# Kernel tuning notes

Hardware: AMD Instinct MI355X
Metric: run time of the kernel (lower is better)

Reference implementation:

```python
import jax, jax.numpy as jnp
import numpy as np

B, S, T, H, V = 32, 64, 64, 512, 32000


def setup_inputs() -> dict:
    key = jax.random.key(0)
    ks = jax.random.split(key, 14)
    enc = jax.random.normal(ks[0], (B, S, H), jnp.float32)
    h0 = jax.random.normal(ks[1], (1, B, H), jnp.float32)
    # encoder padding mask: at least half of each row valid (avoids all -inf rows)
    src_len = jax.random.randint(ks[2], (B,), S // 2, S + 1)
    enc_mask = (jnp.arange(S)[None, :] < src_len[:, None])
    tgt = jax.random.randint(ks[3], (B, T), 0, V)
    fra_len = jax.random.randint(ks[4], (B,), 1, T + 1).at[0].set(T)
    s = 1.0 / np.sqrt(H)
    emb = jax.random.normal(ks[5], (V, H), jnp.float32) * s
    W_ih = jax.random.uniform(ks[6], (3 * H, H), jnp.float32, -s, s)
    W_hh = jax.random.uniform(ks[7], (3 * H, H), jnp.float32, -s, s)
    b_ih = jax.random.uniform(ks[8], (3 * H,), jnp.float32, -s, s)
    b_hh = jax.random.uniform(ks[9], (3 * H,), jnp.float32, -s, s)
    W_cc = jax.random.uniform(ks[10], (H, 2 * H), jnp.float32, -s, s)
    b_cc = jnp.zeros((H,), jnp.float32)
    W_out = jax.random.uniform(ks[11], (V, H), jnp.float32, -s, s)
    b_out = jnp.zeros((V,), jnp.float32)
    return {"all_encoder_hidden_states": enc, "initial_decoder_hidden_state": h0,
            "encoder_output_mask": enc_mask, "target_input": tgt, "fra_length": fra_len,
            "embedding": emb, "W_ih": W_ih, "W_hh": W_hh, "b_ih": b_ih, "b_hh": b_hh,
            "W_cc": W_cc, "b_cc": b_cc, "W_out": W_out, "b_out": b_out}


def reference(all_encoder_hidden_states, initial_decoder_hidden_state, encoder_output_mask,
              target_input, fra_length, embedding, W_ih, W_hh, b_ih, b_hh,
              W_cc, b_cc, W_out, b_out):
    enc = all_encoder_hidden_states            # [B,S,H]
    mask = encoder_output_mask                 # [B,S] bool
    xs = embedding[target_input].transpose(1, 0, 2)  # [T,B,H]
    ts = jnp.arange(xs.shape[0])

    def step(h, inp):                          # h: [B,H]
        x, t = inp
        gx = x @ W_ih.T + b_ih                 # [B,3H]
        gh = h @ W_hh.T + b_hh
        gxr, gxz, gxn = jnp.split(gx, 3, axis=-1)
        ghr, ghz, ghn = jnp.split(gh, 3, axis=-1)
        r = jax.nn.sigmoid(gxr + ghr)
        z = jax.nn.sigmoid(gxz + ghz)
        n = jnp.tanh(gxn + r * ghn)
        h_new = (1.0 - z) * n + z * h          # torch GRU update
        # Luong dot-product attention
        scores = jnp.einsum('bsh,bh->bs', enc, h_new)
        scores = jnp.where(mask, scores, -jnp.inf)
        alphas = jax.nn.softmax(scores, axis=-1)
        ctx = jnp.einsum('bs,bsh->bh', alphas, enc)
        ho = jnp.tanh(jnp.concatenate([ctx, h_new], axis=-1) @ W_cc.T + b_cc)
        logit = ho @ W_out.T + b_out           # [B,V]
        active = (t < fra_length)[:, None]
        h_next = jnp.where(active, h_new, h)   # freeze finished sequences
        return h_next, logit

    _, logits = jax.lax.scan(step, initial_decoder_hidden_state[0], (xs, ts))
    logits = logits.transpose(1, 0, 2)          # [B,T,V]
    return jax.nn.log_softmax(logits, axis=-1)
```

## Files before the change

### kernel.cpp

```cpp
#include <hip/hip_runtime.h>

static constexpr int Bn = 32, Sn = 64, Tn = 64, Hn = 512, Vn = 32000;
static constexpr int H3 = 1536;
static constexpr int NBLK = 64;

typedef __attribute__((ext_vector_type(8))) short bf16x8;
typedef __attribute__((ext_vector_type(4))) float f32x4;

__device__ __forceinline__ short f2bf(float f) {
    unsigned u = __float_as_uint(f);
    u += 0x7FFFu + ((u >> 16) & 1u);
    return (short)(u >> 16);
}
__device__ __forceinline__ float bf2f(short s) {
    return __uint_as_float(((unsigned)(unsigned short)s) << 16);
}

__device__ __forceinline__ void gload16(const void* g, void* l) {
    __builtin_amdgcn_global_load_lds(
        (const __attribute__((address_space(1))) unsigned int*)g,
        (__attribute__((address_space(3))) unsigned int*)l, 16, 0, 0);
}

__global__ __launch_bounds__(128) void k_gather(const int* __restrict__ tgt,
                                                const float* __restrict__ emb,
                                                short* __restrict__ Xb) {
    int m = blockIdx.x;
    int c = threadIdx.x * 4;
    const float4 v = *(const float4*)(emb + (long)tgt[m] * Hn + c);
    short4 o; o.x = f2bf(v.x); o.y = f2bf(v.y); o.z = f2bf(v.z); o.w = f2bf(v.w);
    *(short4*)(Xb + (long)m * Hn + c) = o;
}

__global__ __launch_bounds__(256) void k_cvt(const float* __restrict__ src, int src_ld, int src_off,
                                             short* __restrict__ dst, long total4) {
    for (long i = (long)blockIdx.x * 256 + threadIdx.x; i < total4; i += (long)gridDim.x * 256) {
        long e = i * 4;
        long r = e >> 9; int c = (int)(e & 511);
        const float4 v = *(const float4*)(src + r * (long)src_ld + src_off + c);
        short4 o; o.x = f2bf(v.x); o.y = f2bf(v.y); o.z = f2bf(v.z); o.w = f2bf(v.w);
        *(short4*)(dst + e) = o;
    }
}

__global__ __launch_bounds__(256) void k_gemm_bf16(const short* __restrict__ A, int lda,
                                                   const short* __restrict__ Bm, int ldb,
                                                   const float* __restrict__ bias,
                                                   float* __restrict__ C, int ldc, int K) {
    __shared__ short lA[4096];
    __shared__ short lB[4096];
    const int tid = threadIdx.x;
    const int row0 = blockIdx.y * 128;
    const int col0 = blockIdx.x * 128;
    const int lane = tid & 63;
    const int w = tid >> 6;
    const int wr = w >> 1, wc = w & 1;
    const int g = lane >> 4, rr = lane & 15;

    f32x4 acc[4][4];
    for (int m = 0; m < 4; ++m)
        for (int n = 0; n < 4; ++n)
            for (int q = 0; q < 4; ++q) acc[m][n][q] = 0.f;

    for (int kk = 0; kk < K; kk += 32) {
        for (int p = 0; p < 2; ++p) {
            int u = p * 256 + tid;
            int kg = u >> 7, r = u & 127;
            gload16(A + (long)(row0 + r) * lda + kk + kg * 8, &lA[u * 8]);
            gload16(Bm + (long)(col0 + r) * ldb + kk + kg * 8, &lB[u * 8]);
        }
        __syncthreads();
        bf16x8 av[4], bv[4];
        for (int m = 0; m < 4; ++m)
            av[m] = *(const bf16x8*)&lA[(g * 128 + wr * 64 + m * 16 + rr) * 8];
        for (int n = 0; n < 4; ++n)
            bv[n] = *(const bf16x8*)&lB[(g * 128 + wc * 64 + n * 16 + rr) * 8];
        for (int m = 0; m < 4; ++m)
            for (int n = 0; n < 4; ++n)
                acc[m][n] = __builtin_amdgcn_mfma_f32_16x16x32_bf16(av[m], bv[n], acc[m][n], 0, 0, 0);
        __syncthreads();
    }

    for (int n = 0; n < 4; ++n) {
        int gc = col0 + wc * 64 + n * 16 + rr;
        float bb = bias ? bias[gc] : 0.f;
        for (int m = 0; m < 4; ++m) {
            int gr = row0 + wr * 64 + m * 16 + g * 4;
            for (int q = 0; q < 4; ++q)
                C[(long)(gr + q) * ldc + gc] = acc[m][n][q] + bb;
        }
    }
}

struct WSm2 {
    short h_all[Bn * Hn];
    short hnb[2][Bn * Hn];
    float gh_sl[3 * 16 * 32];
    float y1l[Bn * 16];
    int   flen[Bn];
};
struct BSm2 {
    short encl[Sn * 520];
    short encWl[Sn * Hn];
    float scp[8][64];
    float al[64];
    short hnf[Hn];
};
union USm2 { WSm2 w; BSm2 b; };

__device__ __forceinline__ void sig_flag(unsigned* slot, unsigned val) {
    asm volatile("s_waitcnt vmcnt(0)" ::: "memory");
    __syncthreads();
    if (threadIdx.x == 0)
        __hip_atomic_store(slot, val, __ATOMIC_RELAXED, __HIP_MEMORY_SCOPE_AGENT);
}
__device__ __forceinline__ void wait_flags32(const unsigned* base, unsigned need) {
    if (threadIdx.x < 32) {
        while (__hip_atomic_load(base + threadIdx.x * 32, __ATOMIC_RELAXED, __HIP_MEMORY_SCOPE_AGENT) < need)
            __builtin_amdgcn_s_sleep(1);
    }
    __syncthreads();
}

__global__ __launch_bounds__(512, 1) void k_seq(
    const float* __restrict__ GX, const float* __restrict__ enc,
    const void* __restrict__ maskp, const int* __restrict__ fra,
    const float* __restrict__ h0,
    const short* __restrict__ Whh_b, const float* __restrict__ b_hh,
    const short* __restrict__ Wcc2_b, const float* __restrict__ b_cc,
    const float* __restrict__ encW,
    short* __restrict__ ho_out,
    unsigned long long* __restrict__ hn_pub,
    float* __restrict__ y1_pub,
    unsigned* __restrict__ flags)
{
    __shared__ __align__(16) USm2 sm;
    const int bid = blockIdx.x;
    const int tid = threadIdx.x;
    const int wv = tid >> 6, lane = tid & 63;
    unsigned* flagW = flags;
    unsigned* flagB = flags + 1024;

    if (bid < Bn) {
        bf16x8 afr[16];
        if (wv < 6) {
            const int g = wv >> 1;
            const int row = g * 512 + bid * 16 + (lane & 15);
            #pragma unroll
            for (int k = 0; k < 16; ++k)
                afr[k] = *(const bf16x8*)(Whh_b + (long)row * 512 + k * 32 + (lane >> 4) * 8);
        } else {
            const int row = bid * 16 + (lane & 15);
            #pragma unroll
            for (int k = 0; k < 16; ++k)
                afr[k] = *(const bf16x8*)(Wcc2_b + (long)row * 512 + k * 32 + (lane >> 4) * 8);
        }
        if (tid < Bn) sm.w.flen[tid] = fra[tid];
        #pragma unroll
        for (int it = 0; it < 8; ++it) {
            const int idx2 = it * 512 + tid;
            const int b = idx2 >> 7, ci2 = idx2 & 127;
            const int j0 = ci2 * 4;
            const int soff = b * 512 + ((((ci2 >> 1)) ^ (b & 7)) << 3) + (ci2 & 1) * 4;
            const float4 v = *(const float4*)(h0 + b * 512 + j0);
            unsigned long long pk = (unsigned long long)(unsigned short)f2bf(v.x)
                                  | ((unsigned long long)(unsigned short)f2bf(v.y) << 16)
                                  | ((unsigned long long)(unsigned short)f2bf(v.z) << 32)
                                  | ((unsigned long long)(unsigned short)f2bf(v.w) << 48);
            *(unsigned long long*)&sm.w.h_all[soff] = pk;
        }

        const int eb = tid >> 4, jj = tid & 15;
        float h_carry = h0[eb * 512 + bid * 16 + jj];
        const int flen_e = fra[eb];

        for (int t = 0; t <= Tn + 1; ++t) {
            float gxr = 0.f, gxz = 0.f, gxn = 0.f;
            if (t < Tn) {
                const long base = (long)(eb * Tn + t) * H3 + bid * 16 + jj;
                gxr = GX[base]; gxz = GX[base + 512]; gxn = GX[base + 1024];
            }
            if (t >= 1 && t <= Tn) {
                wait_flags32(flagW, (unsigned)t);
                const unsigned long long* src = hn_pub + ((t - 1) & 1) * 4096;
                short* dst = sm.w.hnb[(t - 1) & 1];
                #pragma unroll
                for (int it = 0; it < 8; ++it) {
                    const int idx2 = it * 512 + tid;
                    const int b = idx2 >> 7, ci2 = idx2 & 127;
                    const int soff = b * 512 + ((((ci2 >> 1)) ^ (b & 7)) << 3) + (ci2 & 1) * 4;
                    const unsigned long long v = __hip_atomic_load(src + idx2, __ATOMIC_RELAXED, __HIP_MEMORY_SCOPE_AGENT);
                    *(unsigned long long*)&dst[soff] = v;
                    if (t - 1 < sm.w.flen[b]) *(unsigned long long*)&sm.w.h_all[soff] = v;
                }
            }
            __syncthreads();
            if (t < Tn && wv < 6) {
                const int g = wv >> 1, n = wv & 1;
                const int bq = n * 16 + (lane & 15);
                f32x4 a0 = {0.f, 0.f, 0.f, 0.f}, a1 = {0.f, 0.f, 0.f, 0.f};
                #pragma unroll
                for (int k = 0; k < 8; ++k) {
                    const int c0 = k * 4 + (lane >> 4);
                    const int c1 = (k + 8) * 4 + (lane >> 4);
                    bf16x8 b0 = *(const bf16x8*)&sm.w.h_all[bq * 512 + ((c0 ^ (bq & 7)) << 3)];
                    bf16x8 b1 = *(const bf16x8*)&sm.w.h_all[bq * 512 + ((c1 ^ (bq & 7)) << 3)];
                    a0 = __builtin_amdgcn_mfma_f32_16x16x32_bf16(afr[k], b0, a0, 0, 0, 0);
                    a1 = __builtin_amdgcn_mfma_f32_16x16x32_bf16(afr[k + 8], b1, a1, 0, 0, 0);
                }
                const int r0 = (lane >> 4) * 4;
                #pragma unroll
                for (int q = 0; q < 4; ++q)
                    sm.w.gh_sl[g * 512 + (r0 + q) * 32 + bq] = a0[q] + a1[q];
            }
            __syncthreads();
            if (t < Tn) {
                const int j = bid * 16 + jj;
                const float ghr = sm.w.gh_sl[jj * 32 + eb]          + b_hh[j];
                const float ghz = sm.w.gh_sl[512 + jj * 32 + eb]    + b_hh[512 + j];
                const float ghn = sm.w.gh_sl[1024 + jj * 32 + eb]   + b_hh[1024 + j];
                const float r = 1.f / (1.f + expf(-(gxr + ghr)));
                const float z = 1.f / (1.f + expf(-(gxz + ghz)));
                const float nn = tanhf(gxn + r * ghn);
                const float hv = (1.f - z) * nn + z * h_carry;
                h_carry = (t < flen_e) ? hv : h_carry;
                int w32 = (int)(unsigned short)f2bf(hv);
                int n1 = __shfl_down(w32, 1);
                int n2 = __shfl_down(w32, 2);
                int n3 = __shfl_down(w32, 3);
                if ((jj & 3) == 0) {
                    unsigned long long pk = (unsigned long long)(unsigned)(w32 | (n1 << 16))
                                          | ((unsigned long long)(unsigned)(n2 | (n3 << 16)) << 32);
                    __hip_atomic_store(hn_pub + (t & 1) * 4096 + eb * 128 + bid * 4 + (jj >> 2), pk,
                                       __ATOMIC_RELAXED, __HIP_MEMORY_SCOPE_AGENT);
                }
                sig_flag(flagW + bid * 32, (unsigned)(t + 1));
            }
            if (t >= 2) {
                wait_flags32(flagB, (unsigned)(t - 1));
                sm.w.y1l[tid] = __hip_atomic_load(
                    y1_pub + ((t - 2) % 3) * (Bn * Hn) + (tid >> 4) * 512 + bid * 16 + (tid & 15),
                    __ATOMIC_RELAXED, __HIP_MEMORY_SCOPE_AGENT);
                __syncthreads();
                if (wv >= 6) {
                    const int n = wv - 6;
                    const int bq = n * 16 + (lane & 15);
                    const short* hsrc = sm.w.hnb[(t - 2) & 1];
                    f32x4 a0 = {0.f, 0.f, 0.f, 0.f}, a1 = {0.f, 0.f, 0.f, 0.f};
                    #pragma unroll
                    for (int k = 0; k < 8; ++k) {
                        const int c0 = k * 4 + (lane >> 4);
                        const int c1 = (k + 8) * 4 + (lane >> 4);
                        bf16x8 b0 = *(const bf16x8*)&hsrc[bq * 512 + ((c0 ^ (bq & 7)) << 3)];
                        bf16x8 b1 = *(const bf16x8*)&hsrc[bq * 512 + ((c1 ^ (bq & 7)) << 3)];
                        a0 = __builtin_amdgcn_mfma_f32_16x16x32_bf16(afr[k], b0, a0, 0, 0, 0);
                        a1 = __builtin_amdgcn_mfma_f32_16x16x32_bf16(afr[k + 8], b1, a1, 0, 0, 0);
                    }
                    const int r0 = (lane >> 4) * 4;
                    short4 o;
                    o.x = f2bf(tanhf(a0[0] + a1[0] + sm.w.y1l[bq * 16 + r0 + 0] + b_cc[bid * 16 + r0 + 0]));
                    o.y = f2bf(tanhf(a0[1] + a1[1] + sm.w.y1l[bq * 16 + r0 + 1] + b_cc[bid * 16 + r0 + 1]));
                    o.z = f2bf(tanhf(a0[2] + a1[2] + sm.w.y1l[bq * 16 + r0 + 2] + b_cc[bid * 16 + r0 + 2]));
                    o.w = f2bf(tanhf(a0[3] + a1[3] + sm.w.y1l[bq * 16 + r0 + 3] + b_cc[bid * 16 + r0 + 3]));
                    *(short4*)(ho_out + ((long)(bq * Tn + (t - 2))) * Hn + bid * 16 + r0) = o;
                }
            }
        }
    } else {
        const int b = bid - Bn;
        const unsigned w0 = ((const unsigned*)maskp)[0];
        const int mmode = (w0 == 1u) ? 0 : (w0 == 0x3F800000u ? 2 : 1);
        {
            const float* encb = enc + (long)b * (Sn * Hn);
            #pragma unroll
            for (int it = 0; it < 16; ++it) {
                int e = (it * 512 + tid) * 4;
                float4 v = *(const float4*)(encb + e);
                int s = e >> 9, k = e & 511;
                short4 o; o.x = f2bf(v.x); o.y = f2bf(v.y); o.z = f2bf(v.z); o.w = f2bf(v.w);
                *(short4*)(sm.b.encl + s * 520 + k) = o;
            }
        }
        {
            const float* ewb = encW + (long)b * (Sn * Hn);
            #pragma unroll
            for (int it = 0; it < 16; ++it) {
                int e = (it * 512 + tid) * 4;
                float4 v = *(const float4*)(ewb + e);
                short4 o; o.x = f2bf(v.x); o.y = f2bf(v.y); o.z = f2bf(v.z); o.w = f2bf(v.w);
                *(short4*)(sm.b.encWl + e) = o;
            }
        }

        for (int u = 0; u < Tn; ++u) {
            wait_flags32(flagW, (unsigned)(u + 1));
            if (tid < 128) {
                unsigned long long v = __hip_atomic_load(hn_pub + (u & 1) * 4096 + b * 128 + tid,
                                                         __ATOMIC_RELAXED, __HIP_MEMORY_SCOPE_AGENT);
                *(unsigned long long*)&sm.b.hnf[tid * 4] = v;
            }
            __syncthreads();
            {
                const int s = tid & 63, sub = tid >> 6;
                const short* erow = sm.b.encl + s * 520 + sub * 64;
                const short* hrow = sm.b.hnf + sub * 64;
                float p = 0.f;
                #pragma unroll
                for (int c8 = 0; c8 < 8; ++c8) {
                    bf16x8 ev = *(const bf16x8*)(erow + c8 * 8);
                    bf16x8 hv8 = *(const bf16x8*)(hrow + c8 * 8);
                    #pragma unroll
                    for (int e = 0; e < 8; ++e)
                        p += bf2f(ev[e]) * bf2f(hv8[e]);
                }
                sm.b.scp[sub][s] = p;
            }
            __syncthreads();
            if (tid < 64) {
                float v = 0.f;
                #pragma unroll
                for (int q = 0; q < 8; ++q) v += sm.b.scp[q][tid];
                bool mv;
                if (mmode == 0)      mv = ((const int*)maskp)[b * Sn + tid] != 0;
                else if (mmode == 1) mv = ((const unsigned char*)maskp)[b * Sn + tid] != 0;
                else                 mv = ((const float*)maskp)[b * Sn + tid] != 0.f;
                v = mv ? v : -__builtin_inff();
                float mx = v;
                for (int o = 1; o < 64; o <<= 1) mx = fmaxf(mx, __shfl_xor(mx, o));
                float e = expf(v - mx);
                float su = e;
                for (int o = 1; o < 64; o <<= 1) su += __shfl_xor(su, o);
                sm.b.al[tid] = e / su;
            }
            __syncthreads();
            {
                float acc = 0.f;
                #pragma unroll 8
                for (int s = 0; s < 64; ++s)
                    acc += sm.b.al[s] * bf2f(sm.b.encWl[s * 512 + tid]);
                __hip_atomic_store(y1_pub + (u % 3) * (Bn * Hn) + b * 512 + tid, acc,
                                   __ATOMIC_RELAXED, __HIP_MEMORY_SCOPE_AGENT);
            }
            sig_flag(flagB + b * 32, (unsigned)(u + 1));
        }
    }
}

__global__ __launch_bounds__(256) void k_logsoftmax(float* __restrict__ out) {
    const long row = blockIdx.x;
    float* p = out + row * (long)Vn;
    const int tid = threadIdx.x;
    __shared__ float redm[4];
    __shared__ float reds[4];

    float mx = -__builtin_inff(), sm = 0.f;
    for (int i = tid; i < Vn / 4; i += 256) {
        float4 v = *(const float4*)(p + i * 4);
        float e0 = v.x, e1 = v.y, e2 = v.z, e3 = v.w;
        float m01 = fmaxf(e0, e1), m23 = fmaxf(e2, e3);
        float ml = fmaxf(m01, m23);
        float nm = fmaxf(mx, ml);
        sm = sm * __expf(mx - nm) + __expf(e0 - nm) + __expf(e1 - nm) + __expf(e2 - nm) + __expf(e3 - nm);
        mx = nm;
    }
    for (int o = 1; o < 64; o <<= 1) {
        float omx = __shfl_xor(mx, o), osm = __shfl_xor(sm, o);
        float nm = fmaxf(mx, omx);
        sm = sm * __expf(mx - nm) + osm * __expf(omx - nm);
        mx = nm;
    }
    if ((tid & 63) == 0) { redm[tid >> 6] = mx; reds[tid >> 6] = sm; }
    __syncthreads();
    float gmx = fmaxf(fmaxf(redm[0], redm[1]), fmaxf(redm[2], redm[3]));
    float gsm = reds[0] * __expf(redm[0] - gmx) + reds[1] * __expf(redm[1] - gmx)
              + reds[2] * __expf(redm[2] - gmx) + reds[3] * __expf(redm[3] - gmx);
    const float lse = gmx + logf(gsm);

    for (int i = tid; i < Vn / 4; i += 256) {
        float4 v = *(const float4*)(p + i * 4);
        v.x -= lse; v.y -= lse; v.z -= lse; v.w -= lse;
        *(float4*)(p + i * 4) = v;
    }
}

extern "C" void kernel_launch(void* const* d_in, const int* in_sizes, int n_in,
                              void* d_out, int out_size, void* d_ws, size_t ws_size,
                              hipStream_t stream) {
    const float* enc   = (const float*)d_in[0];
    const float* h0    = (const float*)d_in[1];
    const void*  maskp = d_in[2];
    const int*   tgt   = (const int*)d_in[3];
    const int*   fra   = (const int*)d_in[4];
    const float* emb   = (const float*)d_in[5];
    const float* W_ih  = (const float*)d_in[6];
    const float* W_hh  = (const float*)d_in[7];
    const float* b_ih  = (const float*)d_in[8];
    const float* b_hh  = (const float*)d_in[9];
    const float* W_cc  = (const float*)d_in[10];
    const float* b_cc  = (const float*)d_in[11];
    const float* W_out = (const float*)d_in[12];
    const float* b_out = (const float*)d_in[13];
    float* out = (float*)d_out;

    char* ws = (char*)d_ws;
    float*    GX      = (float*)ws;   ws += (long)2048 * 1536 * 4;
    float*    encW_ws = (float*)ws;   ws += (long)2048 * 512 * 4;
    short*    Xb      = (short*)ws;   ws += (long)2048 * 512 * 2;
    short*    Wih_b   = (short*)ws;   ws += (long)1536 * 512 * 2;
    short*    Wout_b  = (short*)ws;   ws += (long)32000 * 512 * 2;
    short*    Whh_b   = (short*)ws;   ws += (long)1536 * 512 * 2;
    short*    Wc1_b   = (short*)ws;   ws += (long)512 * 512 * 2;
    short*    Wcc2_b  = (short*)ws;   ws += (long)512 * 512 * 2;
    short*    enc_b   = (short*)ws;   ws += (long)2048 * 512 * 2;
    short*    ho_b    = (short*)ws;   ws += (long)2048 * 512 * 2;
    unsigned long long* hn_pub = (unsigned long long*)ws; ws += (long)2 * 4096 * 8;
    float*    y1_pub  = (float*)ws;   ws += (long)3 * 32 * 512 * 4;
    unsigned* flags   = (unsigned*)ws; ws += 2 * 1024 * 4;

    k_gather<<<2048, 128, 0, stream>>>(tgt, emb, Xb);
    k_cvt<<<768, 256, 0, stream>>>(W_ih, 512, 0, Wih_b, (long)1536 * 512 / 4);
    k_cvt<<<4096, 256, 0, stream>>>(W_out, 512, 0, Wout_b, (long)32000 * 512 / 4);
    k_cvt<<<768, 256, 0, stream>>>(W_hh, 512, 0, Whh_b, (long)1536 * 512 / 4);
    k_cvt<<<256, 256, 0, stream>>>(W_cc, 1024, 0, Wc1_b, (long)512 * 512 / 4);
    k_cvt<<<256, 256, 0, stream>>>(W_cc, 1024, 512, Wcc2_b, (long)512 * 512 / 4);
    k_cvt<<<1024, 256, 0, stream>>>(enc, 512, 0, enc_b, (long)2048 * 512 / 4);

    k_gemm_bf16<<<dim3(12, 16), 256, 0, stream>>>(Xb, 512, Wih_b, 512, b_ih, GX, 1536, 512);
    k_gemm_bf16<<<dim3(4, 16), 256, 0, stream>>>(enc_b, 512, Wc1_b, 512, nullptr, encW_ws, 512, 512);

    hipMemsetAsync(flags, 0, 2 * 1024 * 4, stream);
    k_seq<<<NBLK, 512, 0, stream>>>(GX, enc, maskp, fra, h0,
                                    Whh_b, b_hh, Wcc2_b, b_cc, encW_ws,
                                    ho_b, hn_pub, y1_pub, flags);

    k_gemm_bf16<<<dim3(250, 16), 256, 0, stream>>>(ho_b, 512, Wout_b, 512, b_out, out, 32000, 512);

    k_logsoftmax<<<2048, 256, 0, stream>>>(out);
}
```

Before: 751.0 us.

## Move attention out of the recurrent kernel into batched post-recurrence kernels

```diff
diff --git a/kernel.cpp b/kernel.cpp
--- a/kernel.cpp
+++ b/kernel.cpp
@@ -2,7 +2,6 @@
 
 static constexpr int Bn = 32, Sn = 64, Tn = 64, Hn = 512, Vn = 32000;
 static constexpr int H3 = 1536;
-static constexpr int NBLK = 64;
 
 typedef __attribute__((ext_vector_type(8))) short bf16x8;
 typedef __attribute__((ext_vector_type(4))) float f32x4;
@@ -92,21 +91,57 @@
     }
 }
 
-struct WSm2 {
-    short h_all[Bn * Hn];
-    short hnb[2][Bn * Hn];
-    float gh_sl[3 * 16 * 32];
-    float y1l[Bn * 16];
-    int   flen[Bn];
-};
-struct BSm2 {
-    short encl[Sn * 520];
-    short encWl[Sn * Hn];
-    float scp[8][64];
-    float al[64];
-    short hnf[Hn];
-};
-union USm2 { WSm2 w; BSm2 b; };
+__global__ __launch_bounds__(256) void k_ho(const short* __restrict__ A1, const short* __restrict__ A2,
+                                            const short* __restrict__ B1, const short* __restrict__ B2,
+                                            const float* __restrict__ bias, short* __restrict__ C) {
+    __shared__ short lA[4096];
+    __shared__ short lB[4096];
+    const int tid = threadIdx.x;
+    const int row0 = blockIdx.y * 128;
+    const int col0 = blockIdx.x * 128;
+    const int lane = tid & 63;
+    const int w = tid >> 6;
+    const int wr = w >> 1, wc = w & 1;
+    const int g = lane >> 4, rr = lane & 15;
+
+    f32x4 acc[4][4];
+    for (int m = 0; m < 4; ++m)
+        for (int n = 0; n < 4; ++n)
+            for (int q = 0; q < 4; ++q) acc[m][n][q] = 0.f;
+
+    for (int ph = 0; ph < 2; ++ph) {
+        const short* A = ph ? A2 : A1;
+        const short* Bm = ph ? B2 : B1;
+        for (int kk = 0; kk < 512; kk += 32) {
+            for (int p = 0; p < 2; ++p) {
+                int u = p * 256 + tid;
+                int kg = u >> 7, r = u & 127;
+                gload16(A + (long)(row0 + r) * 512 + kk + kg * 8, &lA[u * 8]);
+                gload16(Bm + (long)(col0 + r) * 512 + kk + kg * 8, &lB[u * 8]);
+            }
+            __syncthreads();
+            bf16x8 av[4], bv[4];
+            for (int m = 0; m < 4; ++m)
+                av[m] = *(const bf16x8*)&lA[(g * 128 + wr * 64 + m * 16 + rr) * 8];
+            for (int n = 0; n < 4; ++n)
+                bv[n] = *(const bf16x8*)&lB[(g * 128 + wc * 64 + n * 16 + rr) * 8];
+            for (int m = 0; m < 4; ++m)
+                for (int n = 0; n < 4; ++n)
+                    acc[m][n] = __builtin_amdgcn_mfma_f32_16x16x32_bf16(av[m], bv[n], acc[m][n], 0, 0, 0);
+            __syncthreads();
+        }
+    }
+
+    for (int n = 0; n < 4; ++n) {
+        int gc = col0 + wc * 64 + n * 16 + rr;
+        float bb = bias[gc];
+        for (int m = 0; m < 4; ++m) {
+            int gr = row0 + wr * 64 + m * 16 + g * 4;
+            for (int q = 0; q < 4; ++q)
+                C[(long)(gr + q) * 512 + gc] = f2bf(tanhf(acc[m][n][q] + bb));
+        }
+    }
+}
 
 __device__ __forceinline__ void sig_flag(unsigned* slot, unsigned val) {
     asm volatile("s_waitcnt vmcnt(0)" ::: "memory");
@@ -123,225 +158,234 @@
 }
 
 __global__ __launch_bounds__(512, 1) void k_seq(
-    const float* __restrict__ GX, const float* __restrict__ enc,
-    const void* __restrict__ maskp, const int* __restrict__ fra,
+    const float* __restrict__ GX, const int* __restrict__ fra,
     const float* __restrict__ h0,
     const short* __restrict__ Whh_b, const float* __restrict__ b_hh,
-    const short* __restrict__ Wcc2_b, const float* __restrict__ b_cc,
-    const float* __restrict__ encW,
-    short* __restrict__ ho_out,
+    short* __restrict__ hn_all,
     unsigned long long* __restrict__ hn_pub,
-    float* __restrict__ y1_pub,
     unsigned* __restrict__ flags)
 {
-    __shared__ __align__(16) USm2 sm;
+    __shared__ __align__(16) short h_all[Bn * Hn];
+    __shared__ float gh_sl[3 * 16 * 32];
+    __shared__ int flen[Bn];
     const int bid = blockIdx.x;
     const int tid = threadIdx.x;
     const int wv = tid >> 6, lane = tid & 63;
-    unsigned* flagW = flags;
-    unsigned* flagB = flags + 1024;
-
-    if (bid < Bn) {
-        bf16x8 afr[16];
+
+    bf16x8 afr[16];
+    if (wv < 6) {
+        const int g = wv >> 1;
+        const int row = g * 512 + bid * 16 + (lane & 15);
+        #pragma unroll
+        for (int k = 0; k < 16; ++k)
+            afr[k] = *(const bf16x8*)(Whh_b + (long)row * 512 + k * 32 + (lane >> 4) * 8);
+    }
+    if (tid < Bn) flen[tid] = fra[tid];
+    #pragma unroll
+    for (int it = 0; it < 8; ++it) {
+        const int idx2 = it * 512 + tid;
+        const int b = idx2 >> 7, ci2 = idx2 & 127;
+        const int j0 = ci2 * 4;
+        const int soff = b * 512 + ((((ci2 >> 1)) ^ (b & 7)) << 3) + (ci2 & 1) * 4;
+        const float4 v = *(const float4*)(h0 + b * 512 + j0);
+        unsigned long long pk = (unsigned long long)(unsigned short)f2bf(v.x)
+                              | ((unsigned long long)(unsigned short)f2bf(v.y) << 16)
+                              | ((unsigned long long)(unsigned short)f2bf(v.z) << 32)
+                              | ((unsigned long long)(unsigned short)f2bf(v.w) << 48);
+        *(unsigned long long*)&h_all[soff] = pk;
+    }
+
+    const int eb = tid >> 4, jj = tid & 15;
+    float h_carry = h0[eb * 512 + bid * 16 + jj];
+    const int flen_e = fra[eb];
+
+    for (int t = 0; t < Tn; ++t) {
+        const long base = (long)(eb * Tn + t) * H3 + bid * 16 + jj;
+        const float gxr = GX[base];
+        const float gxz = GX[base + 512];
+        const float gxn = GX[base + 1024];
+        if (t >= 1) {
+            wait_flags32(flags, (unsigned)t);
+            const unsigned long long* src = hn_pub + ((t - 1) & 1) * 4096;
+            #pragma unroll
+            for (int it = 0; it < 8; ++it) {
+                const int idx2 = it * 512 + tid;
+                const int b = idx2 >> 7, ci2 = idx2 & 127;
+                if (t - 1 < flen[b]) {
+                    const int soff = b * 512 + ((((ci2 >> 1)) ^ (b & 7)) << 3) + (ci2 & 1) * 4;
+                    *(unsigned long long*)&h_all[soff] =
+                        __hip_atomic_load(src + idx2, __ATOMIC_RELAXED, __HIP_MEMORY_SCOPE_AGENT);
+                }
+            }
+        }
+        __syncthreads();
         if (wv < 6) {
-            const int g = wv >> 1;
-            const int row = g * 512 + bid * 16 + (lane & 15);
-            #pragma unroll
-            for (int k = 0; k < 16; ++k)
-                afr[k] = *(const bf16x8*)(Whh_b + (long)row * 512 + k * 32 + (lane >> 4) * 8);
-        } else {
-            const int row = bid * 16 + (lane & 15);
-            #pragma unroll
-            for (int k = 0; k < 16; ++k)
-                afr[k] = *(const bf16x8*)(Wcc2_b + (long)row * 512 + k * 32 + (lane >> 4) * 8);
-        }
-        if (tid < Bn) sm.w.flen[tid] = fra[tid];
+            const int g = wv >> 1, n = wv & 1;
+            const int bq = n * 16 + (lane & 15);
+            f32x4 a0 = {0.f, 0.f, 0.f, 0.f}, a1 = {0.f, 0.f, 0.f, 0.f};
+            #pragma unroll
+            for (int k = 0; k < 8; ++k) {
+                const int c0 = k * 4 + (lane >> 4);
+                const int c1 = (k + 8) * 4 + (lane >> 4);
+                bf16x8 b0 = *(const bf16x8*)&h_all[bq * 512 + ((c0 ^ (bq & 7)) << 3)];
+                bf16x8 b1 = *(const bf16x8*)&h_all[bq * 512 + ((c1 ^ (bq & 7)) << 3)];
+                a0 = __builtin_amdgcn_mfma_f32_16x16x32_bf16(afr[k], b0, a0, 0, 0, 0);
+                a1 = __builtin_amdgcn_mfma_f32_16x16x32_bf16(afr[k + 8], b1, a1, 0, 0, 0);
+            }
+            const int r0 = (lane >> 4) * 4;
+            #pragma unroll
+            for (int q = 0; q < 4; ++q)
+                gh_sl[g * 512 + (r0 + q) * 32 + bq] = a0[q] + a1[q];
+        }
+        __syncthreads();
+        {
+            const int j = bid * 16 + jj;
+            const float ghr = gh_sl[jj * 32 + eb]          + b_hh[j];
+            const float ghz = gh_sl[512 + jj * 32 + eb]    + b_hh[512 + j];
+            const float ghn = gh_sl[1024 + jj * 32 + eb]   + b_hh[1024 + j];
+            const float r = 1.f / (1.f + expf(-(gxr + ghr)));
+            const float z = 1.f / (1.f + expf(-(gxz + ghz)));
+            const float nn = tanhf(gxn + r * ghn);
+            const float hv = (1.f - z) * nn + z * h_carry;
+            h_carry = (t < flen_e) ? hv : h_carry;
+            const short hb = f2bf(hv);
+            int w32 = (int)(unsigned short)hb;
+            int n1 = __shfl_down(w32, 1);
+            int n2 = __shfl_down(w32, 2);
+            int n3 = __shfl_down(w32, 3);
+            if ((jj & 3) == 0) {
+                unsigned long long pk = (unsigned long long)(unsigned)(w32 | (n1 << 16))
+                                      | ((unsigned long long)(unsigned)(n2 | (n3 << 16)) << 32);
+                __hip_atomic_store(hn_pub + (t & 1) * 4096 + eb * 128 + bid * 4 + (jj >> 2), pk,
+                                   __ATOMIC_RELAXED, __HIP_MEMORY_SCOPE_AGENT);
+            }
+            sig_flag(flags + bid * 32, (unsigned)(t + 1));
+            hn_all[(long)(eb * Tn + t) * Hn + bid * 16 + jj] = hb;
+        }
+    }
+}
+
+__global__ __launch_bounds__(512, 1) void k_attn(
+    const float* __restrict__ enc, const short* __restrict__ hn_all,
+    const void* __restrict__ maskp, short* __restrict__ ctx_b)
+{
+    __shared__ __align__(16) short encl[64 * 536];
+    __shared__ __align__(16) short hnlbuf[64 * 536];
+    __shared__ __align__(16) float scl[64 * 64];
+    __shared__ __align__(16) short albc[64 * 72];
+    const int b = blockIdx.x;
+    const int tid = threadIdx.x;
+    const int wv = tid >> 6, lane = tid & 63;
+    const int g = lane >> 4, rr = lane & 15;
+
+    const unsigned w0 = ((const unsigned*)maskp)[0];
+    const int mmode = (w0 == 1u) ? 0 : (w0 == 0x3F800000u ? 2 : 1);
+
+    {
+        const float* encb = enc + (long)b * (Sn * Hn);
+        #pragma unroll
+        for (int it = 0; it < 16; ++it) {
+            int e = (it * 512 + tid) * 4;
+            float4 v = *(const float4*)(encb + e);
+            int s = e >> 9, k = e & 511;
+            short4 o; o.x = f2bf(v.x); o.y = f2bf(v.y); o.z = f2bf(v.z); o.w = f2bf(v.w);
+            *(short4*)(encl + s * 536 + k) = o;
+        }
+    }
+    {
+        const short* hb = hn_all + (long)b * (Tn * Hn);
         #pragma unroll
         for (int it = 0; it < 8; ++it) {
-            const int idx2 = it * 512 + tid;
-            const int b = idx2 >> 7, ci2 = idx2 & 127;
-            const int j0 = ci2 * 4;
-            const int soff = b * 512 + ((((ci2 >> 1)) ^ (b & 7)) << 3) + (ci2 & 1) * 4;
-            const float4 v = *(const float4*)(h0 + b * 512 + j0);
-            unsigned long long pk = (unsigned long long)(unsigned short)f2bf(v.x)
-                                  | ((unsigned long long)(unsigned short)f2bf(v.y) << 16)
-                                  | ((unsigned long long)(unsigned short)f2bf(v.z) << 32)
-                                  | ((unsigned long long)(unsigned short)f2bf(v.w) << 48);
-            *(unsigned long long*)&sm.w.h_all[soff] = pk;
-        }
-
-        const int eb = tid >> 4, jj = tid & 15;
-        float h_carry = h0[eb * 512 + bid * 16 + jj];
-        const int flen_e = fra[eb];
-
-        for (int t = 0; t <= Tn + 1; ++t) {
-            float gxr = 0.f, gxz = 0.f, gxn = 0.f;
-            if (t < Tn) {
-                const long base = (long)(eb * Tn + t) * H3 + bid * 16 + jj;
-                gxr = GX[base]; gxz = GX[base + 512]; gxn = GX[base + 1024];
-            }
-            if (t >= 1 && t <= Tn) {
-                wait_flags32(flagW, (unsigned)t);
-                const unsigned long long* src = hn_pub + ((t - 1) & 1) * 4096;
-                short* dst = sm.w.hnb[(t - 1) & 1];
-                #pragma unroll
-                for (int it = 0; it < 8; ++it) {
-                    const int idx2 = it * 512 + tid;
-                    const int b = idx2 >> 7, ci2 = idx2 & 127;
-                    const int soff = b * 512 + ((((ci2 >> 1)) ^ (b & 7)) << 3) + (ci2 & 1) * 4;
-                    const unsigned long long v = __hip_atomic_load(src + idx2, __ATOMIC_RELAXED, __HIP_MEMORY_SCOPE_AGENT);
-                    *(unsigned long long*)&dst[soff] = v;
-                    if (t - 1 < sm.w.flen[b]) *(unsigned long long*)&sm.w.h_all[soff] = v;
-                }
-            }
-            __syncthreads();
-            if (t < Tn && wv < 6) {
-                const int g = wv >> 1, n = wv & 1;
-                const int bq = n * 16 + (lane & 15);
-                f32x4 a0 = {0.f, 0.f, 0.f, 0.f}, a1 = {0.f, 0.f, 0.f, 0.f};
-                #pragma unroll
-                for (int k = 0; k < 8; ++k) {
-                    const int c0 = k * 4 + (lane >> 4);
-                    const int c1 = (k + 8) * 4 + (lane >> 4);
-                    bf16x8 b0 = *(const bf16x8*)&sm.w.h_all[bq * 512 + ((c0 ^ (bq & 7)) << 3)];
-                    bf16x8 b1 = *(const bf16x8*)&sm.w.h_all[bq * 512 + ((c1 ^ (bq & 7)) << 3)];
-                    a0 = __builtin_amdgcn_mfma_f32_16x16x32_bf16(afr[k], b0, a0, 0, 0, 0);
-                    a1 = __builtin_amdgcn_mfma_f32_16x16x32_bf16(afr[k + 8], b1, a1, 0, 0, 0);
-                }
-                const int r0 = (lane >> 4) * 4;
-                #pragma unroll
-                for (int q = 0; q < 4; ++q)
-                    sm.w.gh_sl[g * 512 + (r0 + q) * 32 + bq] = a0[q] + a1[q];
-            }
-            __syncthreads();
-            if (t < Tn) {
-                const int j = bid * 16 + jj;
-                const float ghr = sm.w.gh_sl[jj * 32 + eb]          + b_hh[j];
-                const float ghz = sm.w.gh_sl[512 + jj * 32 + eb]    + b_hh[512 + j];
-                const float ghn = sm.w.gh_sl[1024 + jj * 32 + eb]   + b_hh[1024 + j];
-                const float r = 1.f / (1.f + expf(-(gxr + ghr)));
-                const float z = 1.f / (1.f + expf(-(gxz + ghz)));
-                const float nn = tanhf(gxn + r * ghn);
-                const float hv = (1.f - z) * nn + z * h_carry;
-                h_carry = (t < flen_e) ? hv : h_carry;
-                int w32 = (int)(unsigned short)f2bf(hv);
-                int n1 = __shfl_down(w32, 1);
-                int n2 = __shfl_down(w32, 2);
-                int n3 = __shfl_down(w32, 3);
-                if ((jj & 3) == 0) {
-                    unsigned long long pk = (unsigned long long)(unsigned)(w32 | (n1 << 16))
-                                          | ((unsigned long long)(unsigned)(n2 | (n3 << 16)) << 32);
-                    __hip_atomic_store(hn_pub + (t & 1) * 4096 + eb * 128 + bid * 4 + (jj >> 2), pk,
-                                       __ATOMIC_RELAXED, __HIP_MEMORY_SCOPE_AGENT);
-                }
-                sig_flag(flagW + bid * 32, (unsigned)(t + 1));
-            }
-            if (t >= 2) {
-                wait_flags32(flagB, (unsigned)(t - 1));
-                sm.w.y1l[tid] = __hip_atomic_load(
-                    y1_pub + ((t - 2) % 3) * (Bn * Hn) + (tid >> 4) * 512 + bid * 16 + (tid & 15),
-                    __ATOMIC_RELAXED, __HIP_MEMORY_SCOPE_AGENT);
-                __syncthreads();
-                if (wv >= 6) {
-                    const int n = wv - 6;
-                    const int bq = n * 16 + (lane & 15);
-                    const short* hsrc = sm.w.hnb[(t - 2) & 1];
-                    f32x4 a0 = {0.f, 0.f, 0.f, 0.f}, a1 = {0.f, 0.f, 0.f, 0.f};
-                    #pragma unroll
-                    for (int k = 0; k < 8; ++k) {
-                        const int c0 = k * 4 + (lane >> 4);
-                        const int c1 = (k + 8) * 4 + (lane >> 4);
-                        bf16x8 b0 = *(const bf16x8*)&hsrc[bq * 512 + ((c0 ^ (bq & 7)) << 3)];
-                        bf16x8 b1 = *(const bf16x8*)&hsrc[bq * 512 + ((c1 ^ (bq & 7)) << 3)];
-                        a0 = __builtin_amdgcn_mfma_f32_16x16x32_bf16(afr[k], b0, a0, 0, 0, 0);
-                        a1 = __builtin_amdgcn_mfma_f32_16x16x32_bf16(afr[k + 8], b1, a1, 0, 0, 0);
-                    }
-                    const int r0 = (lane >> 4) * 4;
-                    short4 o;
-                    o.x = f2bf(tanhf(a0[0] + a1[0] + sm.w.y1l[bq * 16 + r0 + 0] + b_cc[bid * 16 + r0 + 0]));
-                    o.y = f2bf(tanhf(a0[1] + a1[1] + sm.w.y1l[bq * 16 + r0 + 1] + b_cc[bid * 16 + r0 + 1]));
-                    o.z = f2bf(tanhf(a0[2] + a1[2] + sm.w.y1l[bq * 16 + r0 + 2] + b_cc[bid * 16 + r0 + 2]));
-                    o.w = f2bf(tanhf(a0[3] + a1[3] + sm.w.y1l[bq * 16 + r0 + 3] + b_cc[bid * 16 + r0 + 3]));
-                    *(short4*)(ho_out + ((long)(bq * Tn + (t - 2))) * Hn + bid * 16 + r0) = o;
-                }
-            }
-        }
-    } else {
-        const int b = bid - Bn;
-        const unsigned w0 = ((const unsigned*)maskp)[0];
-        const int mmode = (w0 == 1u) ? 0 : (w0 == 0x3F800000u ? 2 : 1);
-        {
-            const float* encb = enc + (long)b * (Sn * Hn);
-            #pragma unroll
-            for (int it = 0; it < 16; ++it) {
-                int e = (it * 512 + tid) * 4;
-                float4 v = *(const float4*)(encb + e);
-                int s = e >> 9, k = e & 511;
-                short4 o; o.x = f2bf(v.x); o.y = f2bf(v.y); o.z = f2bf(v.z); o.w = f2bf(v.w);
-                *(short4*)(sm.b.encl + s * 520 + k) = o;
-            }
-        }
-        {
-            const float* ewb = encW + (long)b * (Sn * Hn);
-            #pragma unroll
-            for (int it = 0; it < 16; ++it) {
-                int e = (it * 512 + tid) * 4;
-                float4 v = *(const float4*)(ewb + e);
-                short4 o; o.x = f2bf(v.x); o.y = f2bf(v.y); o.z = f2bf(v.z); o.w = f2bf(v.w);
-                *(short4*)(sm.b.encWl + e) = o;
-            }
-        }
-
-        for (int u = 0; u < Tn; ++u) {
-            wait_flags32(flagW, (unsigned)(u + 1));
-            if (tid < 128) {
-                unsigned long long v = __hip_atomic_load(hn_pub + (u & 1) * 4096 + b * 128 + tid,
-                                                         __ATOMIC_RELAXED, __HIP_MEMORY_SCOPE_AGENT);
-                *(unsigned long long*)&sm.b.hnf[tid * 4] = v;
-            }
-            __syncthreads();
-            {
-                const int s = tid & 63, sub = tid >> 6;
-                const short* erow = sm.b.encl + s * 520 + sub * 64;
-                const short* hrow = sm.b.hnf + sub * 64;
-                float p = 0.f;
-                #pragma unroll
-                for (int c8 = 0; c8 < 8; ++c8) {
-                    bf16x8 ev = *(const bf16x8*)(erow + c8 * 8);
-                    bf16x8 hv8 = *(const bf16x8*)(hrow + c8 * 8);
-                    #pragma unroll
-                    for (int e = 0; e < 8; ++e)
-                        p += bf2f(ev[e]) * bf2f(hv8[e]);
-                }
-                sm.b.scp[sub][s] = p;
-            }
-            __syncthreads();
-            if (tid < 64) {
-                float v = 0.f;
-                #pragma unroll
-                for (int q = 0; q < 8; ++q) v += sm.b.scp[q][tid];
-                bool mv;
-                if (mmode == 0)      mv = ((const int*)maskp)[b * Sn + tid] != 0;
-                else if (mmode == 1) mv = ((const unsigned char*)maskp)[b * Sn + tid] != 0;
-                else                 mv = ((const float*)maskp)[b * Sn + tid] != 0.f;
-                v = mv ? v : -__builtin_inff();
-                float mx = v;
-                for (int o = 1; o < 64; o <<= 1) mx = fmaxf(mx, __shfl_xor(mx, o));
-                float e = expf(v - mx);
-                float su = e;
-                for (int o = 1; o < 64; o <<= 1) su += __shfl_xor(su, o);
-                sm.b.al[tid] = e / su;
-            }
-            __syncthreads();
-            {
-                float acc = 0.f;
-                #pragma unroll 8
-                for (int s = 0; s < 64; ++s)
-                    acc += sm.b.al[s] * bf2f(sm.b.encWl[s * 512 + tid]);
-                __hip_atomic_store(y1_pub + (u % 3) * (Bn * Hn) + b * 512 + tid, acc,
-                                   __ATOMIC_RELAXED, __HIP_MEMORY_SCOPE_AGENT);
-            }
-            sig_flag(flagB + b * 32, (unsigned)(u + 1));
+            int u = it * 512 + tid;
+            int t = u >> 6, k8 = (u & 63) * 8;
+            *(int4*)(hnlbuf + t * 536 + k8) = *(const int4*)(hb + t * 512 + k8);
+        }
+    }
+    __syncthreads();
+
+    for (int i = 0; i < 2; ++i) {
+        const int id = wv * 2 + i;
+        const int tt = id >> 2, ss = id & 3;
+        f32x4 a0 = {0.f, 0.f, 0.f, 0.f}, a1 = {0.f, 0.f, 0.f, 0.f};
+        #pragma unroll
+        for (int k = 0; k < 8; ++k) {
+            bf16x8 av0 = *(const bf16x8*)&hnlbuf[(tt * 16 + rr) * 536 + k * 32 + g * 8];
+            bf16x8 bv0 = *(const bf16x8*)&encl[(ss * 16 + rr) * 536 + k * 32 + g * 8];
+            bf16x8 av1 = *(const bf16x8*)&hnlbuf[(tt * 16 + rr) * 536 + (k + 8) * 32 + g * 8];
+            bf16x8 bv1 = *(const bf16x8*)&encl[(ss * 16 + rr) * 536 + (k + 8) * 32 + g * 8];
+            a0 = __builtin_amdgcn_mfma_f32_16x16x32_bf16(av0, bv0, a0, 0, 0, 0);
+            a1 = __builtin_amdgcn_mfma_f32_16x16x32_bf16(av1, bv1, a1, 0, 0, 0);
+        }
+        #pragma unroll
+        for (int q = 0; q < 4; ++q)
+            scl[(tt * 16 + g * 4 + q) * 64 + ss * 16 + rr] = a0[q] + a1[q];
+    }
+    __syncthreads();
+
+    {
+        const int t = wv * 8 + (lane >> 3);
+        const int sub = lane & 7;
+        float v[8];
+        #pragma unroll
+        for (int e = 0; e < 8; ++e) {
+            const int s = sub * 8 + e;
+            bool mv;
+            if (mmode == 0)      mv = ((const int*)maskp)[b * Sn + s] != 0;
+            else if (mmode == 1) mv = ((const unsigned char*)maskp)[b * Sn + s] != 0;
+            else                 mv = ((const float*)maskp)[b * Sn + s] != 0.f;
+            v[e] = mv ? scl[t * 64 + s] : -__builtin_inff();
+        }
+        float mx = v[0];
+        #pragma unroll
+        for (int e = 1; e < 8; ++e) mx = fmaxf(mx, v[e]);
+        mx = fmaxf(mx, __shfl_xor(mx, 1));
+        mx = fmaxf(mx, __shfl_xor(mx, 2));
+        mx = fmaxf(mx, __shfl_xor(mx, 4));
+        float su = 0.f;
+        float ev[8];
+        #pragma unroll
+        for (int e = 0; e < 8; ++e) { ev[e] = __expf(v[e] - mx); su += ev[e]; }
+        su += __shfl_xor(su, 1);
+        su += __shfl_xor(su, 2);
+        su += __shfl_xor(su, 4);
+        const float inv = 1.f / su;
+        bf16x8 o;
+        #pragma unroll
+        for (int e = 0; e < 8; ++e) o[e] = f2bf(ev[e] * inv);
+        *(bf16x8*)&albc[t * 72 + sub * 8] = o;
+    }
+    {
+        short* enct = hnlbuf;
+        const int j = tid;
+        #pragma unroll
+        for (int c = 0; c < 8; ++c) {
+            bf16x8 tmp;
+            #pragma unroll
+            for (int e = 0; e < 8; ++e) tmp[e] = encl[(c * 8 + e) * 536 + j];
+            *(bf16x8*)&enct[j * 64 + ((c ^ (j & 7)) * 8)] = tmp;
+        }
+    }
+    __syncthreads();
+
+    {
+        const short* enct = hnlbuf;
+        for (int i = 0; i < 16; ++i) {
+            const int id = wv * 16 + i;
+            const int tt = id >> 5, jt = id & 31;
+            const int jr = jt * 16 + rr;
+            f32x4 acc = {0.f, 0.f, 0.f, 0.f};
+            #pragma unroll
+            for (int kk = 0; kk < 2; ++kk) {
+                bf16x8 av = *(const bf16x8*)&albc[(tt * 16 + rr) * 72 + kk * 32 + g * 8];
+                const int c = kk * 4 + g;
+                bf16x8 bv = *(const bf16x8*)&enct[jr * 64 + ((c ^ (jr & 7)) * 8)];
+                acc = __builtin_amdgcn_mfma_f32_16x16x32_bf16(av, bv, acc, 0, 0, 0);
+            }
+            #pragma unroll
+            for (int q = 0; q < 4; ++q) {
+                const int t = tt * 16 + g * 4 + q;
+                ctx_b[(long)(b * Tn + t) * Hn + jr] = f2bf(acc[q]);
+            }
         }
     }
 }
@@ -356,11 +400,9 @@
     float mx = -__builtin_inff(), sm = 0.f;
     for (int i = tid; i < Vn / 4; i += 256) {
         float4 v = *(const float4*)(p + i * 4);
-        float e0 = v.x, e1 = v.y, e2 = v.z, e3 = v.w;
-        float m01 = fmaxf(e0, e1), m23 = fmaxf(e2, e3);
-        float ml = fmaxf(m01, m23);
+        float ml = fmaxf(fmaxf(v.x, v.y), fmaxf(v.z, v.w));
         float nm = fmaxf(mx, ml);
-        sm = sm * __expf(mx - nm) + __expf(e0 - nm) + __expf(e1 - nm) + __expf(e2 - nm) + __expf(e3 - nm);
+        sm = sm * __expf(mx - nm) + __expf(v.x - nm) + __expf(v.y - nm) + __expf(v.z - nm) + __expf(v.w - nm);
         mx = nm;
     }
     for (int o = 1; o < 64; o <<= 1) {
@@ -404,18 +446,17 @@
 
     char* ws = (char*)d_ws;
     float*    GX      = (float*)ws;   ws += (long)2048 * 1536 * 4;
-    float*    encW_ws = (float*)ws;   ws += (long)2048 * 512 * 4;
     short*    Xb      = (short*)ws;   ws += (long)2048 * 512 * 2;
     short*    Wih_b   = (short*)ws;   ws += (long)1536 * 512 * 2;
     short*    Wout_b  = (short*)ws;   ws += (long)32000 * 512 * 2;
     short*    Whh_b   = (short*)ws;   ws += (long)1536 * 512 * 2;
     short*    Wc1_b   = (short*)ws;   ws += (long)512 * 512 * 2;
     short*    Wcc2_b  = (short*)ws;   ws += (long)512 * 512 * 2;
-    short*    enc_b   = (short*)ws;   ws += (long)2048 * 512 * 2;
     short*    ho_b    = (short*)ws;   ws += (long)2048 * 512 * 2;
+    short*    hn_all  = (short*)ws;   ws += (long)2048 * 512 * 2;
+    short*    ctx_b   = (short*)ws;   ws += (long)2048 * 512 * 2;
     unsigned long long* hn_pub = (unsigned long long*)ws; ws += (long)2 * 4096 * 8;
-    float*    y1_pub  = (float*)ws;   ws += (long)3 * 32 * 512 * 4;
-    unsigned* flags   = (unsigned*)ws; ws += 2 * 1024 * 4;
+    unsigned* flags   = (unsigned*)ws; ws += 1024 * 4;
 
     k_gather<<<2048, 128, 0, stream>>>(tgt, emb, Xb);
     k_cvt<<<768, 256, 0, stream>>>(W_ih, 512, 0, Wih_b, (long)1536 * 512 / 4);
@@ -423,15 +464,15 @@
     k_cvt<<<768, 256, 0, stream>>>(W_hh, 512, 0, Whh_b, (long)1536 * 512 / 4);
     k_cvt<<<256, 256, 0, stream>>>(W_cc, 1024, 0, Wc1_b, (long)512 * 512 / 4);
     k_cvt<<<256, 256, 0, stream>>>(W_cc, 1024, 512, Wcc2_b, (long)512 * 512 / 4);
-    k_cvt<<<1024, 256, 0, stream>>>(enc, 512, 0, enc_b, (long)2048 * 512 / 4);
 
     k_gemm_bf16<<<dim3(12, 16), 256, 0, stream>>>(Xb, 512, Wih_b, 512, b_ih, GX, 1536, 512);
-    k_gemm_bf16<<<dim3(4, 16), 256, 0, stream>>>(enc_b, 512, Wc1_b, 512, nullptr, encW_ws, 512, 512);
-
-    hipMemsetAsync(flags, 0, 2 * 1024 * 4, stream);
-    k_seq<<<NBLK, 512, 0, stream>>>(GX, enc, maskp, fra, h0,
-                                    Whh_b, b_hh, Wcc2_b, b_cc, encW_ws,
-                                    ho_b, hn_pub, y1_pub, flags);
+
+    hipMemsetAsync(flags, 0, 1024 * 4, stream);
+    k_seq<<<32, 512, 0, stream>>>(GX, fra, h0, Whh_b, b_hh, hn_all, hn_pub, flags);
+
+    k_attn<<<32, 512, 0, stream>>>(enc, hn_all, maskp, ctx_b);
+
+    k_ho<<<dim3(4, 16), 256, 0, stream>>>(ctx_b, hn_all, Wc1_b, Wcc2_b, b_cc, ho_b);
 
     k_gemm_bf16<<<dim3(250, 16), 256, 0, stream>>>(ho_b, 512, Wout_b, 512, b_out, out, 32000, 512);
 
```

Result: faster. 689.1 us (-8.2%).
